# Performance work log

Hardware: AMD Instinct MI355X
Metric: run time of the kernel (lower is better)

Reference implementation:

```python
import jax, jax.numpy as jnp
import numpy as np

DIV_COEF = 1.0
EPS = 1e-8  # torch.cosine_similarity default eps


def setup_inputs() -> dict:
    key = jax.random.key(0)
    id_ = jax.random.normal(key, (8192, 512), dtype=jnp.float32)
    return {"id": id_}


def reference(id):
    # cosine similarity via norm + GEMM (math identical to broadcast form)
    norms = jnp.linalg.norm(id, axis=1)                      # [N]
    dots = id @ id.T                                          # [N, N]
    sim = dots / jnp.maximum(norms[:, None] * norms[None, :], EPS)
    n = id.shape[0]
    # zero diagonal, clamp negatives to zero, mean over full NxN
    off_diag = 1.0 - jnp.eye(n, dtype=sim.dtype)
    id_sim = off_diag * sim
    l_id_div = jnp.mean(jnp.where(id_sim < 0, 0.0, id_sim))
    total_loss = DIV_COEF * l_id_div
    return (total_loss, l_id_div)
```

## Files before the change

kernel.cpp:

```cpp
#include <hip/hip_runtime.h>
#include <stdint.h>

#define NROWS 8192
#define KDIM  512
#define BM    128
#define BK    128
#define NKI   (KDIM / BK)
#define NT    (NROWS / BM)
#define NBLK  (NT * (NT + 1) / 2)

typedef __attribute__((ext_vector_type(4))) float f32x4;
typedef long i64;

__device__ __forceinline__ void async_copy16(const unsigned char* g, unsigned char* l) {
  __builtin_amdgcn_global_load_lds(
      (const __attribute__((address_space(1))) unsigned int*)g,
      (__attribute__((address_space(3))) unsigned int*)l,
      16, 0, 0);
}

__global__ __launch_bounds__(256) void prep_kernel(
    const float* __restrict__ src, unsigned char* __restrict__ dst,
    float* __restrict__ acc) {
  const int row  = blockIdx.x * 4 + (threadIdx.x >> 6);
  const int lane = threadIdx.x & 63;
  const float4 v0 = ((const float4*)src)[row * 128 + lane * 2];
  const float4 v1 = ((const float4*)src)[row * 128 + lane * 2 + 1];
  float ss = v0.x * v0.x + v0.y * v0.y + v0.z * v0.z + v0.w * v0.w
           + v1.x * v1.x + v1.y * v1.y + v1.z * v1.z + v1.w * v1.w;
  #pragma unroll
  for (int off = 32; off > 0; off >>= 1) ss += __shfl_down(ss, off);
  const float rn = 1.0f / sqrtf(__shfl(ss, 0));
  if (row == 0 && lane == 0) *acc = 0.0f;
  int pk0 = __builtin_amdgcn_cvt_pk_fp8_f32(v0.x * rn, v0.y * rn, 0, false);
  pk0     = __builtin_amdgcn_cvt_pk_fp8_f32(v0.z * rn, v0.w * rn, pk0, true);
  int pk1 = __builtin_amdgcn_cvt_pk_fp8_f32(v1.x * rn, v1.y * rn, 0, false);
  pk1     = __builtin_amdgcn_cvt_pk_fp8_f32(v1.z * rn, v1.w * rn, pk1, true);
  const int cg  = lane >> 1;
  const int win = cg >> 3;
  const int p   = (cg & 7) ^ (row & 7);
  const int hf  = (lane & 1) ^ ((row >> 3) & 1);
  uint2 o; o.x = (unsigned int)pk0; o.y = (unsigned int)pk1;
  ((uint2*)dst)[row * 64 + win * 16 + p * 2 + hf] = o;
}

__device__ __forceinline__ int tri_base(int b) {
  return b * NT - (b * (b - 1)) / 2;
}

__global__ __launch_bounds__(256) void sim_reduce_kernel(
    const unsigned char* __restrict__ idn, float* __restrict__ acc) {
  const int idx = blockIdx.x;
  const float Af = 2.0f * NT + 1.0f;
  int bi = (int)((Af - sqrtf(Af * Af - 8.0f * (float)idx)) * 0.5f);
  while (bi > 0 && tri_base(bi) > idx) bi--;
  while (tri_base(bi + 1) <= idx) bi++;
  const int bj = bi + (idx - tri_base(bi));

  __shared__ __align__(16) unsigned char As[2][BM * BK];
  __shared__ __align__(16) unsigned char Bs[2][BM * BK];

  const int tid  = threadIdx.x;
  const int lane = tid & 63;
  const int w    = tid >> 6;
  const int wr   = (w >> 1) * 64;
  const int wc   = (w & 1) * 64;
  const int q    = lane >> 4;
  const int r16  = lane & 15;
  const int rx   = r16 & 7;
  const int hq   = ((q & 1) ^ ((r16 >> 3) & 1)) * 8;

  f32x4 acc_f[4][4];
  #pragma unroll
  for (int i = 0; i < 4; i++)
    #pragma unroll
    for (int j = 0; j < 4; j++)
      acc_f[i][j] = (f32x4){0.f, 0.f, 0.f, 0.f};

  const unsigned char* gA = idn + (size_t)(bi * BM + (tid >> 3)) * KDIM + (tid & 7) * 16;
  const unsigned char* gB = idn + (size_t)(bj * BM + (tid >> 3)) * KDIM + (tid & 7) * 16;
  const int ldso = tid * 16;

  #pragma unroll
  for (int i = 0; i < 4; i++) async_copy16(gA + (size_t)i * 16384, &As[0][ldso + i * 4096]);
  #pragma unroll
  for (int i = 0; i < 4; i++) async_copy16(gB + (size_t)i * 16384, &Bs[0][ldso + i * 4096]);

  #pragma unroll
  for (int t = 0; t < NKI; ++t) {
    const int cs = t & 1;
    if (t + 1 < NKI) {
      const int ns = cs ^ 1;
      const int ko = (t + 1) * BK;
      #pragma unroll
      for (int i = 0; i < 4; i++)
        async_copy16(gA + ko + (size_t)i * 16384, &As[ns][ldso + i * 4096]);
      #pragma unroll
      for (int i = 0; i < 4; i++)
        async_copy16(gB + ko + (size_t)i * 16384, &Bs[ns][ldso + i * 4096]);
      asm volatile("s_waitcnt vmcnt(8)" ::: "memory");
    } else {
      asm volatile("s_waitcnt vmcnt(0)" ::: "memory");
    }
    asm volatile("s_barrier" ::: "memory");

    #pragma unroll
    for (int s = 0; s < 4; s++) {
      const int pos = ((2 * s + (q >> 1)) ^ rx) * 16 + hq;
      i64 a[4], b[4];
      #pragma unroll
      for (int mi = 0; mi < 4; mi++) {
        a[mi] = *(const i64*)&As[cs][(wr + mi * 16 + r16) * BK + pos];
        b[mi] = *(const i64*)&Bs[cs][(wc + mi * 16 + r16) * BK + pos];
      }
      #pragma unroll
      for (int mi = 0; mi < 4; mi++)
        #pragma unroll
        for (int ni = 0; ni < 4; ni++)
          acc_f[mi][ni] = __builtin_amdgcn_mfma_f32_16x16x32_fp8_fp8(
              a[mi], b[ni], acc_f[mi][ni], 0, 0, 0);
    }

    asm volatile("s_barrier" ::: "memory");
  }

  float local = 0.f;
  const bool diag = (bi == bj);
  #pragma unroll
  for (int mi = 0; mi < 4; mi++)
    #pragma unroll
    for (int ni = 0; ni < 4; ni++)
      #pragma unroll
      for (int rr = 0; rr < 4; rr++) {
        const int ri = wr + mi * 16 + q * 4 + rr;
        const int ci = wc + ni * 16 + r16;
        float v = fmaxf(acc_f[mi][ni][rr], 0.f);
        if (diag && ri == ci) v = 0.f;
        local += v;
      }

  #pragma unroll
  for (int off = 32; off > 0; off >>= 1) local += __shfl_down(local, off);
  __syncthreads();
  float* red = (float*)As;
  if (lane == 0) red[w] = local;
  __syncthreads();
  if (tid == 0) {
    float s = red[0] + red[1] + red[2] + red[3];
    if (!diag) s *= 2.f;
    atomicAdd(acc, s);
  }
}

__global__ void finalize_kernel(const float* __restrict__ acc, float* __restrict__ out) {
  const float m = *acc * (1.0f / ((float)NROWS * (float)NROWS));
  out[0] = m;
  out[1] = m;
}

extern "C" void kernel_launch(void* const* d_in, const int* in_sizes, int n_in,
                              void* d_out, int out_size, void* d_ws, size_t ws_size,
                              hipStream_t stream) {
  const float* id = (const float*)d_in[0];
  float* out = (float*)d_out;
  unsigned char* idn = (unsigned char*)d_ws;
  float* acc = (float*)((char*)d_ws + (size_t)NROWS * KDIM);

  prep_kernel<<<NROWS / 4, 256, 0, stream>>>(id, idn, acc);
  sim_reduce_kernel<<<NBLK, 256, 0, stream>>>(idn, acc);
  finalize_kernel<<<1, 1, 0, stream>>>(acc, out);
}
```

Measured before the change: 99.38 us.

## Switch to 32x32x64 scaled FP8 MFMA with matching LDS swizzle

Replaces the 16x16x32 FP8 MFMA tiling with the gfx950 mfma_scale 32x32x64 f8f6f4 instruction, using unit scales. Each wave now issues 4 larger MFMAs per 128-wide k-step instead of 16 small ones, and reads 128-bit LDS fragments. The prep-kernel swizzle is simplified to match the new fragment layout. The aim is higher MFMA throughput and fewer LDS reads, at the risk of new bank conflicts or a fragment layout mismatch that would change results.

```diff
diff --git a/kernel.cpp b/kernel.cpp
--- a/kernel.cpp
+++ b/kernel.cpp
@@ -9,8 +9,9 @@
 #define NT    (NROWS / BM)
 #define NBLK  (NT * (NT + 1) / 2)
 
-typedef __attribute__((ext_vector_type(4))) float f32x4;
-typedef long i64;
+typedef __attribute__((ext_vector_type(4)))  int   i32x4;
+typedef __attribute__((ext_vector_type(8)))  int   i32x8;
+typedef __attribute__((ext_vector_type(16))) float f32x16;
 
 __device__ __forceinline__ void async_copy16(const unsigned char* g, unsigned char* l) {
   __builtin_amdgcn_global_load_lds(
@@ -39,7 +40,7 @@
   const int cg  = lane >> 1;
   const int win = cg >> 3;
   const int p   = (cg & 7) ^ (row & 7);
-  const int hf  = (lane & 1) ^ ((row >> 3) & 1);
+  const int hf  = lane & 1;
   uint2 o; o.x = (unsigned int)pk0; o.y = (unsigned int)pk1;
   ((uint2*)dst)[row * 64 + win * 16 + p * 2 + hf] = o;
 }
@@ -65,17 +66,17 @@
   const int w    = tid >> 6;
   const int wr   = (w >> 1) * 64;
   const int wc   = (w & 1) * 64;
-  const int q    = lane >> 4;
-  const int r16  = lane & 15;
-  const int rx   = r16 & 7;
-  const int hq   = ((q & 1) ^ ((r16 >> 3) & 1)) * 8;
+  const int r32  = lane & 31;
+  const int h    = lane >> 5;
+  const int rx   = r32 & 7;
 
-  f32x4 acc_f[4][4];
+  f32x16 acc_f[2][2];
   #pragma unroll
-  for (int i = 0; i < 4; i++)
+  for (int i = 0; i < 2; i++)
     #pragma unroll
-    for (int j = 0; j < 4; j++)
-      acc_f[i][j] = (f32x4){0.f, 0.f, 0.f, 0.f};
+    for (int j = 0; j < 2; j++)
+      acc_f[i][j] = (f32x16){0.f, 0.f, 0.f, 0.f, 0.f, 0.f, 0.f, 0.f,
+                             0.f, 0.f, 0.f, 0.f, 0.f, 0.f, 0.f, 0.f};
 
   const unsigned char* gA = idn + (size_t)(bi * BM + (tid >> 3)) * KDIM + (tid & 7) * 16;
   const unsigned char* gB = idn + (size_t)(bj * BM + (tid >> 3)) * KDIM + (tid & 7) * 16;
@@ -105,20 +106,31 @@
     asm volatile("s_barrier" ::: "memory");
 
     #pragma unroll
-    for (int s = 0; s < 4; s++) {
-      const int pos = ((2 * s + (q >> 1)) ^ rx) * 16 + hq;
-      i64 a[4], b[4];
+    for (int ks = 0; ks < 2; ks++) {
+      const int c0 = 4 * ks + 2 * h;
+      const int p0 = ((c0)     ^ rx) * 16;
+      const int p1 = ((c0 + 1) ^ rx) * 16;
+      i32x8 af[2], bf[2];
       #pragma unroll
-      for (int mi = 0; mi < 4; mi++) {
-        a[mi] = *(const i64*)&As[cs][(wr + mi * 16 + r16) * BK + pos];
-        b[mi] = *(const i64*)&Bs[cs][(wc + mi * 16 + r16) * BK + pos];
+      for (int mi = 0; mi < 2; mi++) {
+        const unsigned char* ab = &As[cs][(wr + mi * 32 + r32) * BK];
+        const i32x4 alo = *(const i32x4*)(ab + p0);
+        const i32x4 ahi = *(const i32x4*)(ab + p1);
+        af[mi] = __builtin_shufflevector(alo, ahi, 0, 1, 2, 3, 4, 5, 6, 7);
+        const unsigned char* bb = &Bs[cs][(wc + mi * 32 + r32) * BK];
+        const i32x4 blo = *(const i32x4*)(bb + p0);
+        const i32x4 bhi = *(const i32x4*)(bb + p1);
+        bf[mi] = __builtin_shufflevector(blo, bhi, 0, 1, 2, 3, 4, 5, 6, 7);
       }
       #pragma unroll
-      for (int mi = 0; mi < 4; mi++)
+      for (int mi = 0; mi < 2; mi++)
         #pragma unroll
-        for (int ni = 0; ni < 4; ni++)
-          acc_f[mi][ni] = __builtin_amdgcn_mfma_f32_16x16x32_fp8_fp8(
-              a[mi], b[ni], acc_f[mi][ni], 0, 0, 0);
+        for (int ni = 0; ni < 2; ni++)
+          acc_f[mi][ni] = __builtin_amdgcn_mfma_scale_f32_32x32x64_f8f6f4(
+              af[mi], bf[ni], acc_f[mi][ni],
+              0, 0,
+              0, 0x7F7F7F7Fu,
+              0, 0x7F7F7F7Fu);
     }
 
     asm volatile("s_barrier" ::: "memory");
@@ -127,14 +139,14 @@
   float local = 0.f;
   const bool diag = (bi == bj);
   #pragma unroll
-  for (int mi = 0; mi < 4; mi++)
+  for (int mi = 0; mi < 2; mi++)
     #pragma unroll
-    for (int ni = 0; ni < 4; ni++)
+    for (int ni = 0; ni < 2; ni++)
       #pragma unroll
-      for (int rr = 0; rr < 4; rr++) {
-        const int ri = wr + mi * 16 + q * 4 + rr;
-        const int ci = wc + ni * 16 + r16;
-        float v = fmaxf(acc_f[mi][ni][rr], 0.f);
+      for (int rg = 0; rg < 16; rg++) {
+        const int ri = wr + mi * 32 + (rg & 3) + 8 * (rg >> 2) + 4 * h;
+        const int ci = wc + ni * 32 + r32;
+        float v = fmaxf(acc_f[mi][ni][rg], 0.f);
         if (diag && ri == ci) v = 0.f;
         local += v;
       }
```

Measured after the change: 100.8 us. Within noise of the previous version (+1.5%).
